# Performance work log

Measured on AMD Instinct MI355X. Metric: run time of the kernel, lower is better.

Reference implementation:

```python
import jax, jax.numpy as jnp
import numpy as np

N = 20000        # nodes
E = 640000       # edges (before self-loops)
F_IN = 128
HID = 64
HEADS = 4
F_OUT = 128
G = 64           # graphs in batch
NEG_SLOPE = 0.2  # PyG GATConv leaky_relu default


def setup_inputs() -> dict:
    key = jax.random.key(0)
    ks = jax.random.split(key, 16)
    s = 0.05
    x = jax.random.normal(ks[0], (N, F_IN), jnp.float32)
    edge_index = jax.random.randint(ks[1], (2, E), 0, N, dtype=jnp.int64)
    batch = jnp.sort(jax.random.randint(ks[2], (N,), 0, G, dtype=jnp.int64))
    # layer 1: F_IN -> HID x HEADS (concat)
    W1 = jax.random.normal(ks[3], (F_IN, HEADS * HID), jnp.float32) * s
    a_src1 = jax.random.normal(ks[4], (HEADS, HID), jnp.float32) * s
    a_dst1 = jax.random.normal(ks[5], (HEADS, HID), jnp.float32) * s
    b1 = jnp.zeros((HEADS * HID,), jnp.float32)
    # layer 2: HEADS*HID -> HID x HEADS (concat)
    W2 = jax.random.normal(ks[6], (HEADS * HID, HEADS * HID), jnp.float32) * s
    a_src2 = jax.random.normal(ks[7], (HEADS, HID), jnp.float32) * s
    a_dst2 = jax.random.normal(ks[8], (HEADS, HID), jnp.float32) * s
    b2 = jnp.zeros((HEADS * HID,), jnp.float32)
    # layer 3: HEADS*HID -> F_OUT, heads=1, concat=False (mean)
    W3 = jax.random.normal(ks[9], (HEADS * HID, F_OUT), jnp.float32) * s
    a_src3 = jax.random.normal(ks[10], (1, F_OUT), jnp.float32) * s
    a_dst3 = jax.random.normal(ks[11], (1, F_OUT), jnp.float32) * s
    b3 = jnp.zeros((F_OUT,), jnp.float32)
    return dict(x=x, edge_index=edge_index, batch=batch,
                W1=W1, a_src1=a_src1, a_dst1=a_dst1, b1=b1,
                W2=W2, a_src2=a_src2, a_dst2=a_dst2, b2=b2,
                W3=W3, a_src3=a_src3, a_dst3=a_dst3, b3=b3)


def _gat_layer(x, src, dst, W, a_s, a_d, b, heads, concat):
    n = x.shape[0]
    h = (x @ W).reshape(n, heads, -1)                # [N,H,C]
    alpha_s = (h * a_s[None]).sum(-1)                # [N,H]
    alpha_d = (h * a_d[None]).sum(-1)                # [N,H]
    e = jax.nn.leaky_relu(alpha_s[src] + alpha_d[dst], NEG_SLOPE)  # [E,H]
    # segment softmax over incoming edges of each dst node
    m = jax.ops.segment_max(e, dst, num_segments=n)
    ex = jnp.exp(e - m[dst])
    denom = jax.ops.segment_sum(ex, dst, num_segments=n)
    alpha = ex / (denom[dst] + 1e-16)                # [E,H]
    out = jax.ops.segment_sum(alpha[:, :, None] * h[src], dst, num_segments=n)  # [N,H,C]
    out = out.reshape(n, -1) if concat else out.mean(axis=1)
    return out + b


def reference(x, edge_index, batch, W1, a_src1, a_dst1, b1,
              W2, a_src2, a_dst2, b2, W3, a_src3, a_dst3, b3):
    n = x.shape[0]
    # add self loops (PyG GATConv default add_self_loops=True)
    loop = jnp.arange(n, dtype=edge_index.dtype)
    src = jnp.concatenate([edge_index[0], loop])
    dst = jnp.concatenate([edge_index[1], loop])

    h = _gat_layer(x, src, dst, W1, a_src1, a_dst1, b1, HEADS, True)
    h = jax.nn.elu(h)
    h = _gat_layer(h, src, dst, W2, a_src2, a_dst2, b2, HEADS, True)
    h = jax.nn.elu(h)
    h = _gat_layer(h, src, dst, W3, a_src3, a_dst3, b3, 1, False)

    # global mean pool over graphs
    sums = jax.ops.segment_sum(h, batch, num_segments=G)
    cnts = jax.ops.segment_sum(jnp.ones((n, 1), h.dtype), batch, num_segments=G)
    graph_embedding = sums / jnp.maximum(cnts, 1.0)
    return graph_embedding, h
```

## Files before the change

### kernel.cpp

```cpp
#include <hip/hip_runtime.h>
#include <hip/hip_bf16.h>
#include <math.h>

#define N_NODES 20000
#define N_EDGES 640000
#define ET_EDGES (N_EDGES + N_NODES)
#define G_GRAPHS 64
#define NEG_SLOPE 0.2f


__global__ void hist_dst(const int* __restrict__ ei, int* __restrict__ cnt,
                         const int* __restrict__ batch, int* __restrict__ gstart) {
    int j = blockIdx.x * blockDim.x + threadIdx.x;
    if (blockIdx.x == 0 && threadIdx.x <= G_GRAPHS) {
        int g = threadIdx.x;
        int lo = 0, hi = N_NODES;
        while (lo < hi) {
            int mid = (lo + hi) >> 1;
            if (batch[mid] < g) lo = mid + 1; else hi = mid;
        }
        gstart[g] = lo;
    }
    if (j >= ET_EDGES) return;
    int d = (j < N_EDGES) ? ei[N_EDGES + j] : (j - N_EDGES);
    atomicAdd(&cnt[d], 1);
}

__global__ __launch_bounds__(1024) void scan_rowptr(const int* __restrict__ cnt,
                                                    int* __restrict__ row_ptr) {
    __shared__ int sums[1024];
    const int n = N_NODES;
    const int CH = (n + 1023) / 1024;
    int t = threadIdx.x;
    int base = t * CH;
    int s = 0;
    for (int i = 0; i < CH; ++i) {
        int idx = base + i;
        if (idx < n) s += cnt[idx];
    }
    sums[t] = s;
    __syncthreads();
    for (int o = 1; o < 1024; o <<= 1) {
        int v = (t >= o) ? sums[t - o] : 0;
        __syncthreads();
        sums[t] += v;
        __syncthreads();
    }
    int run = (t == 0) ? 0 : sums[t - 1];
    for (int i = 0; i < CH; ++i) {
        int idx = base + i;
        if (idx < n) { row_ptr[idx] = run; run += cnt[idx]; }
    }
    if (t == 1023) row_ptr[n] = sums[1023];
}

__global__ void fill_csr(const int* __restrict__ ei, const int* __restrict__ row_ptr,
                         int* __restrict__ cur, int* __restrict__ col) {
    int j = blockIdx.x * blockDim.x + threadIdx.x;
    if (j >= ET_EDGES) return;
    int s, d;
    if (j < N_EDGES) { s = ei[j]; d = ei[N_EDGES + j]; }
    else             { s = d = j - N_EDGES; }
    int pos = row_ptr[d] + atomicAdd(&cur[d], 1);
    col[pos] = s;
}


__global__ __launch_bounds__(256) void sgemm64(const float* __restrict__ A,
                                               const float* __restrict__ B,
                                               float* __restrict__ C,
                                               int M, int K, int Nc) {
    __shared__ float As[16][64];
    __shared__ float Bs[16][64];
    int bm = blockIdx.x * 64;
    int bn = blockIdx.y * 64;
    int t = threadIdx.x;
    int tr = t >> 2, tq = t & 3;
    int bkr = t >> 4, bnq = t & 15;
    int tm = (t >> 4) * 4;
    int tn = (t & 15) * 4;
    float acc[4][4] = {};
    for (int k0 = 0; k0 < K; k0 += 16) {
        int ar = bm + tr;
        float4 av = make_float4(0.f, 0.f, 0.f, 0.f);
        if (ar < M) av = *(const float4*)&A[(size_t)ar * K + k0 + tq * 4];
        As[tq * 4 + 0][tr] = av.x;
        As[tq * 4 + 1][tr] = av.y;
        As[tq * 4 + 2][tr] = av.z;
        As[tq * 4 + 3][tr] = av.w;
        float4 bv = *(const float4*)&B[(size_t)(k0 + bkr) * Nc + bn + bnq * 4];
        *(float4*)&Bs[bkr][bnq * 4] = bv;
        __syncthreads();
        #pragma unroll
        for (int k = 0; k < 16; ++k) {
            float a[4], b[4];
            *(float4*)a = *(const float4*)&As[k][tm];
            *(float4*)b = *(const float4*)&Bs[k][tn];
            #pragma unroll
            for (int i = 0; i < 4; ++i)
                #pragma unroll
                for (int j = 0; j < 4; ++j)
                    acc[i][j] = fmaf(a[i], b[j], acc[i][j]);
        }
        __syncthreads();
    }
    #pragma unroll
    for (int i = 0; i < 4; ++i) {
        int r = bm + tm + i;
        if (r < M) {
            float4 o = make_float4(acc[i][0], acc[i][1], acc[i][2], acc[i][3]);
            *(float4*)&C[(size_t)r * Nc + bn + tn] = o;
        }
    }
}


template <int HEADS, int C>
__global__ __launch_bounds__(256) void node_alpha2(const float* __restrict__ h,
                                                   const float* __restrict__ a_src,
                                                   const float* __restrict__ a_dst,
                                                   float* __restrict__ asT,
                                                   float* __restrict__ adT) {
    constexpr int F = HEADS * C;
    constexpr int VEC = F / 64;
    constexpr int LPH = C / VEC;
    int wid = threadIdx.x >> 6, lane = threadIdx.x & 63;
    int v = blockIdx.x * 4 + wid;
    if (v >= N_NODES) return;
    const float* hp = h + (size_t)v * F + lane * VEC;
    float ps = 0.f, pd = 0.f;
    #pragma unroll
    for (int c = 0; c < VEC; ++c) {
        float hv = hp[c];
        ps = fmaf(hv, a_src[lane * VEC + c], ps);
        pd = fmaf(hv, a_dst[lane * VEC + c], pd);
    }
    #pragma unroll
    for (int o = LPH / 2; o; o >>= 1) {
        ps += __shfl_xor(ps, o);
        pd += __shfl_xor(pd, o);
    }
    if ((lane & (LPH - 1)) == 0) {
        int head = lane / LPH;
        asT[head * N_NODES + v] = ps;
        adT[head * N_NODES + v] = pd;
    }
}


template <int NSLICE, int SCH, int F, int HEADS, bool DO_ELU>
__global__ __launch_bounds__(256) void gat_aggregate_sliced(
        const float* __restrict__ h,
        const float* __restrict__ asT,
        const float* __restrict__ adT,
        const int* __restrict__ row_ptr,
        const int* __restrict__ col,
        const float* __restrict__ bias,
        float* __restrict__ out) {
    constexpr int CL = SCH / 4;
    constexpr int E  = 64 / CL;
    constexpr int CPH = F / HEADS;
    __shared__ int   s_off[4][64];
    __shared__ float s_p[4][64];
    int slice = blockIdx.x & (NSLICE - 1);
    int ng = blockIdx.x >> 2;
    int wid = threadIdx.x >> 6, lane = threadIdx.x & 63;
    int v = ng * 4 + wid;
    if (v >= N_NODES) return;
    int head = (slice * SCH) / CPH;
    int eg = lane / CL, cl = lane % CL;
    int r0 = row_ptr[v], r1 = row_ptr[v + 1];
    float ad = adT[head * N_NODES + v];
    const float* asrc = asT + head * N_NODES;
    float acc[4] = {};
    float lsum = 0.f;
    const char* hb = (const char*)(h + slice * SCH + cl * 4);

    for (int base = r0; base < r1; base += 64) {
        int j = base + lane;
        bool valid = j < r1;
        int s = col[valid ? j : r0];
        float e = asrc[s] + ad;
        e = (e > 0.f) ? e : NEG_SLOPE * e;
        float p = valid ? __expf(e) : 0.f;
        lsum += p;
        s_p[wid][lane] = p;
        s_off[wid][lane] = s * (F * 4);

        int nk = min(64, r1 - base);
        int nkg = (nk + E - 1) / E;
        for (int g = 0; g < nkg; ++g) {
            int k = g * E + eg;
            float pk = s_p[wid][k];
            int off = s_off[wid][k];
            float4 hv = *(const float4*)(hb + off);
            acc[0] = fmaf(pk, hv.x, acc[0]);
            acc[1] = fmaf(pk, hv.y, acc[1]);
            acc[2] = fmaf(pk, hv.z, acc[2]);
            acc[3] = fmaf(pk, hv.w, acc[3]);
        }
    }
    #pragma unroll
    for (int o = 32; o; o >>= 1) lsum += __shfl_xor(lsum, o);
    #pragma unroll
    for (int c = 0; c < 4; ++c) {
        #pragma unroll
        for (int o = CL; o < 64; o <<= 1) acc[c] += __shfl_xor(acc[c], o);
    }
    if (eg == 0) {
        float inv = 1.f / (lsum + 1e-16f);
        #pragma unroll
        for (int c = 0; c < 4; ++c) {
            int ch = slice * SCH + cl * 4 + c;
            float o = acc[c] * inv + bias[ch];
            if (DO_ELU) o = (o > 0.f) ? o : expm1f(o);
            out[(size_t)v * F + ch] = o;
        }
    }
}


__global__ void pool_mean4(const float* __restrict__ hout, const int* __restrict__ gstart,
                           float* __restrict__ gout) {
    int g = blockIdx.x;
    int q = blockIdx.y;
    int c = threadIdx.x;
    int off = gstart[g], end = gstart[g + 1];
    float inv = 1.f / fmaxf((float)(end - off), 1.0f);
    float s = 0.f;
    for (int i = off + q; i < end; i += 4) s += hout[(size_t)i * 128 + c];
    atomicAdd(&gout[g * 128 + c], s * inv);
}


static inline size_t align_up(size_t x, size_t a) { return (x + a - 1) & ~(a - 1); }

extern "C" void kernel_launch(void* const* d_in, const int* in_sizes, int n_in,
                              void* d_out, int out_size, void* d_ws, size_t ws_size,
                              hipStream_t stream) {
    const float* x   = (const float*)d_in[0];
    const int*   ei  = (const int*)d_in[1];
    const int*   bat = (const int*)d_in[2];
    const float* W1  = (const float*)d_in[3];
    const float* as1 = (const float*)d_in[4];
    const float* ad1 = (const float*)d_in[5];
    const float* b1  = (const float*)d_in[6];
    const float* W2  = (const float*)d_in[7];
    const float* as2 = (const float*)d_in[8];
    const float* ad2 = (const float*)d_in[9];
    const float* b2  = (const float*)d_in[10];
    const float* W3  = (const float*)d_in[11];
    const float* as3 = (const float*)d_in[12];
    const float* ad3 = (const float*)d_in[13];
    const float* b3  = (const float*)d_in[14];

    float* gout = (float*)d_out;
    float* hout = (float*)d_out + G_GRAPHS * 128;

    char* w = (char*)d_ws;
    size_t o = 0;
    float* bufA = (float*)(w + o); o = align_up(o + (size_t)N_NODES * 256 * 4, 256);
    float* bufB = (float*)(w + o); o = align_up(o + (size_t)N_NODES * 256 * 4, 256);
    float* asv  = (float*)(w + o); o = align_up(o + (size_t)N_NODES * 4 * 4, 256);
    float* adv  = (float*)(w + o); o = align_up(o + (size_t)N_NODES * 4 * 4, 256);
    int* row_ptr = (int*)(w + o);  o = align_up(o + (size_t)(N_NODES + 1) * 4, 256);
    int* col     = (int*)(w + o);  o = align_up(o + (size_t)ET_EDGES * 4, 256);
    int* cnt     = (int*)(w + o);  o += (size_t)N_NODES * 4;
    int* cur     = (int*)(w + o);  o = align_up(o + (size_t)N_NODES * 4, 256);
    int* gstart  = (int*)(w + o);  o = align_up(o + (size_t)(G_GRAPHS + 1) * 4, 256);

    hipMemsetAsync(cnt, 0, (size_t)N_NODES * 8, stream);
    hipMemsetAsync(gout, 0, (size_t)G_GRAPHS * 128 * 4, stream);
    hist_dst<<<(ET_EDGES + 255) / 256, 256, 0, stream>>>(ei, cnt, bat, gstart);
    scan_rowptr<<<1, 1024, 0, stream>>>(cnt, row_ptr);
    fill_csr<<<(ET_EDGES + 255) / 256, 256, 0, stream>>>(ei, row_ptr, cur, col);

    dim3 g4(313, 4), g2(313, 2);
    int nb = (N_NODES + 3) / 4;
    int nbs = nb * 4;

    sgemm64<<<g4, 256, 0, stream>>>(x, W1, bufA, N_NODES, 128, 256);
    node_alpha2<4, 64><<<nb, 256, 0, stream>>>(bufA, as1, ad1, asv, adv);
    gat_aggregate_sliced<4, 64, 256, 4, true><<<nbs, 256, 0, stream>>>(
        bufA, asv, adv, row_ptr, col, b1, bufB);

    sgemm64<<<g4, 256, 0, stream>>>(bufB, W2, bufA, N_NODES, 256, 256);
    node_alpha2<4, 64><<<nb, 256, 0, stream>>>(bufA, as2, ad2, asv, adv);
    gat_aggregate_sliced<4, 64, 256, 4, true><<<nbs, 256, 0, stream>>>(
        bufA, asv, adv, row_ptr, col, b2, bufB);

    sgemm64<<<g2, 256, 0, stream>>>(bufB, W3, bufA, N_NODES, 256, 128);
    node_alpha2<1, 128><<<nb, 256, 0, stream>>>(bufA, as3, ad3, asv, adv);
    gat_aggregate_sliced<4, 32, 128, 1, false><<<nbs, 256, 0, stream>>>(
        bufA, asv, adv, row_ptr, col, b3, hout);

    pool_mean4<<<dim3(G_GRAPHS, 4), 128, 0, stream>>>(hout, gstart, gout);
}
```

Before: 485.3 us.

## Precompute per-edge attention weights in separate kernel and unroll aggregation loop

Adds an edge_alpha kernel that computes the exp attention scores per edge and head once, storing them and per-node denominators in new buffers. The aggregation kernel then reads the precomputed weights instead of recomputing them in every slice. It also drops the shared-memory staging, unrolls the gather loop four edges deep for more memory-level parallelism, doubles slices to 8, and pre-shifts column indices into byte offsets. In exchange it adds an extra kernel launch and an extra ~10MB write and read of edge weights per layer.

```diff
diff --git a/kernel.cpp b/kernel.cpp
--- a/kernel.cpp
+++ b/kernel.cpp
@@ -55,14 +55,14 @@
 }
 
 __global__ void fill_csr(const int* __restrict__ ei, const int* __restrict__ row_ptr,
-                         int* __restrict__ cur, int* __restrict__ col) {
+                         int* __restrict__ cur, int* __restrict__ colb) {
     int j = blockIdx.x * blockDim.x + threadIdx.x;
     if (j >= ET_EDGES) return;
     int s, d;
     if (j < N_EDGES) { s = ei[j]; d = ei[N_EDGES + j]; }
     else             { s = d = j - N_EDGES; }
     int pos = row_ptr[d] + atomicAdd(&cur[d], 1);
-    col[pos] = s;
+    colb[pos] = s << 10;
 }
 
 
@@ -116,11 +116,11 @@
 
 
 template <int HEADS, int C>
-__global__ __launch_bounds__(256) void node_alpha2(const float* __restrict__ h,
+__global__ __launch_bounds__(256) void node_alpha3(const float* __restrict__ h,
                                                    const float* __restrict__ a_src,
                                                    const float* __restrict__ a_dst,
-                                                   float* __restrict__ asT,
-                                                   float* __restrict__ adT) {
+                                                   float* __restrict__ asi,
+                                                   float* __restrict__ adi) {
     constexpr int F = HEADS * C;
     constexpr int VEC = F / 64;
     constexpr int LPH = C / VEC;
@@ -142,80 +142,139 @@
     }
     if ((lane & (LPH - 1)) == 0) {
         int head = lane / LPH;
-        asT[head * N_NODES + v] = ps;
-        adT[head * N_NODES + v] = pd;
-    }
-}
-
-
-template <int NSLICE, int SCH, int F, int HEADS, bool DO_ELU>
-__global__ __launch_bounds__(256) void gat_aggregate_sliced(
+        asi[v * HEADS + head] = ps;
+        adi[v * HEADS + head] = pd;
+    }
+}
+
+
+template <int H>
+__global__ __launch_bounds__(256) void edge_alpha(
+        const float* __restrict__ asi,
+        const float* __restrict__ adi,
+        const int* __restrict__ row_ptr,
+        const int* __restrict__ colb,
+        float* __restrict__ p,
+        float* __restrict__ dn) {
+    constexpr int KE = 64 / H;
+    constexpr int SHIFT = (H == 4) ? 6 : 8;
+    int wid = threadIdx.x >> 6, lane = threadIdx.x & 63;
+    int v = blockIdx.x * 4 + wid;
+    if (v >= N_NODES) return;
+    int k = lane / H, h = lane % H;
+    int r0 = row_ptr[v], r1 = row_ptr[v + 1];
+    float ad = adi[v * H + h];
+    const char* ab = (const char*)asi + h * 4;
+    float dsum = 0.f;
+    for (int base = r0; base < r1; base += KE) {
+        int j = base + k;
+        bool valid = j < r1;
+        int cb = colb[valid ? j : r0];
+        float as = *(const float*)(ab + (cb >> SHIFT));
+        float e = as + ad;
+        e = (e > 0.f) ? e : NEG_SLOPE * e;
+        float pe = __expf(e);
+        if (valid) {
+            dsum += pe;
+            p[(size_t)j * H + h] = pe;
+        }
+    }
+    #pragma unroll
+    for (int o = H; o < 64; o <<= 1) dsum += __shfl_xor(dsum, o);
+    if (k == 0) dn[v * H + h] = dsum;
+}
+
+
+template <int NSLICE, int SCH, int F, int H, int SHIFT, bool DO_ELU>
+__global__ __launch_bounds__(256) void gat_aggregate3(
         const float* __restrict__ h,
-        const float* __restrict__ asT,
-        const float* __restrict__ adT,
+        const float* __restrict__ p,
+        const float* __restrict__ dn,
         const int* __restrict__ row_ptr,
-        const int* __restrict__ col,
+        const int* __restrict__ colb,
         const float* __restrict__ bias,
         float* __restrict__ out) {
     constexpr int CL = SCH / 4;
     constexpr int E  = 64 / CL;
-    constexpr int CPH = F / HEADS;
-    __shared__ int   s_off[4][64];
-    __shared__ float s_p[4][64];
+    constexpr int CPH = F / H;
     int slice = blockIdx.x & (NSLICE - 1);
-    int ng = blockIdx.x >> 2;
+    int ng = blockIdx.x / NSLICE;
     int wid = threadIdx.x >> 6, lane = threadIdx.x & 63;
     int v = ng * 4 + wid;
     if (v >= N_NODES) return;
     int head = (slice * SCH) / CPH;
     int eg = lane / CL, cl = lane % CL;
     int r0 = row_ptr[v], r1 = row_ptr[v + 1];
-    float ad = adT[head * N_NODES + v];
-    const float* asrc = asT + head * N_NODES;
+    const char* hb = (const char*)(h + slice * SCH + cl * 4);
+    const float* pp = p + head;
     float acc[4] = {};
-    float lsum = 0.f;
-    const char* hb = (const char*)(h + slice * SCH + cl * 4);
-
-    for (int base = r0; base < r1; base += 64) {
-        int j = base + lane;
-        bool valid = j < r1;
-        int s = col[valid ? j : r0];
-        float e = asrc[s] + ad;
-        e = (e > 0.f) ? e : NEG_SLOPE * e;
-        float p = valid ? __expf(e) : 0.f;
-        lsum += p;
-        s_p[wid][lane] = p;
-        s_off[wid][lane] = s * (F * 4);
-
-        int nk = min(64, r1 - base);
-        int nkg = (nk + E - 1) / E;
-        for (int g = 0; g < nkg; ++g) {
-            int k = g * E + eg;
-            float pk = s_p[wid][k];
-            int off = s_off[wid][k];
-            float4 hv = *(const float4*)(hb + off);
-            acc[0] = fmaf(pk, hv.x, acc[0]);
-            acc[1] = fmaf(pk, hv.y, acc[1]);
-            acc[2] = fmaf(pk, hv.z, acc[2]);
-            acc[3] = fmaf(pk, hv.w, acc[3]);
-        }
-    }
-    #pragma unroll
-    for (int o = 32; o; o >>= 1) lsum += __shfl_xor(lsum, o);
+
+    int e0 = r0;
+    for (; e0 + E * 4 <= r1; e0 += E * 4) {
+        int ea = e0 + eg, eb = ea + E, ec = eb + E, ed = ec + E;
+        int oa = colb[ea] >> SHIFT;
+        int ob = colb[eb] >> SHIFT;
+        int oc = colb[ec] >> SHIFT;
+        int od = colb[ed] >> SHIFT;
+        float pa = pp[(size_t)ea * H];
+        float pb = pp[(size_t)eb * H];
+        float pc = pp[(size_t)ec * H];
+        float pd = pp[(size_t)ed * H];
+        float4 ha = *(const float4*)(hb + oa);
+        float4 hc0 = *(const float4*)(hb + ob);
+        float4 hc1 = *(const float4*)(hb + oc);
+        float4 hc2 = *(const float4*)(hb + od);
+        acc[0] = fmaf(pa, ha.x, acc[0]);
+        acc[1] = fmaf(pa, ha.y, acc[1]);
+        acc[2] = fmaf(pa, ha.z, acc[2]);
+        acc[3] = fmaf(pa, ha.w, acc[3]);
+        acc[0] = fmaf(pb, hc0.x, acc[0]);
+        acc[1] = fmaf(pb, hc0.y, acc[1]);
+        acc[2] = fmaf(pb, hc0.z, acc[2]);
+        acc[3] = fmaf(pb, hc0.w, acc[3]);
+        acc[0] = fmaf(pc, hc1.x, acc[0]);
+        acc[1] = fmaf(pc, hc1.y, acc[1]);
+        acc[2] = fmaf(pc, hc1.z, acc[2]);
+        acc[3] = fmaf(pc, hc1.w, acc[3]);
+        acc[0] = fmaf(pd, hc2.x, acc[0]);
+        acc[1] = fmaf(pd, hc2.y, acc[1]);
+        acc[2] = fmaf(pd, hc2.z, acc[2]);
+        acc[3] = fmaf(pd, hc2.w, acc[3]);
+    }
+    for (; e0 < r1; e0 += E) {
+        int e = e0 + eg;
+        bool valid = e < r1;
+        int ee = valid ? e : r0;
+        int oa = colb[ee] >> SHIFT;
+        float pa = pp[(size_t)ee * H];
+        if (!valid) pa = 0.f;
+        float4 ha = *(const float4*)(hb + oa);
+        acc[0] = fmaf(pa, ha.x, acc[0]);
+        acc[1] = fmaf(pa, ha.y, acc[1]);
+        acc[2] = fmaf(pa, ha.z, acc[2]);
+        acc[3] = fmaf(pa, ha.w, acc[3]);
+    }
+
     #pragma unroll
     for (int c = 0; c < 4; ++c) {
         #pragma unroll
         for (int o = CL; o < 64; o <<= 1) acc[c] += __shfl_xor(acc[c], o);
     }
     if (eg == 0) {
-        float inv = 1.f / (lsum + 1e-16f);
-        #pragma unroll
-        for (int c = 0; c < 4; ++c) {
-            int ch = slice * SCH + cl * 4 + c;
-            float o = acc[c] * inv + bias[ch];
-            if (DO_ELU) o = (o > 0.f) ? o : expm1f(o);
-            out[(size_t)v * F + ch] = o;
-        }
+        float inv = 1.f / (dn[v * H + head] + 1e-16f);
+        int ch = slice * SCH + cl * 4;
+        float4 o;
+        o.x = acc[0] * inv + bias[ch + 0];
+        o.y = acc[1] * inv + bias[ch + 1];
+        o.z = acc[2] * inv + bias[ch + 2];
+        o.w = acc[3] * inv + bias[ch + 3];
+        if (DO_ELU) {
+            o.x = (o.x > 0.f) ? o.x : expm1f(o.x);
+            o.y = (o.y > 0.f) ? o.y : expm1f(o.y);
+            o.z = (o.z > 0.f) ? o.z : expm1f(o.z);
+            o.w = (o.w > 0.f) ? o.w : expm1f(o.w);
+        }
+        *(float4*)&out[(size_t)v * F + ch] = o;
     }
 }
 
@@ -263,8 +322,10 @@
     float* bufB = (float*)(w + o); o = align_up(o + (size_t)N_NODES * 256 * 4, 256);
     float* asv  = (float*)(w + o); o = align_up(o + (size_t)N_NODES * 4 * 4, 256);
     float* adv  = (float*)(w + o); o = align_up(o + (size_t)N_NODES * 4 * 4, 256);
+    float* pbuf = (float*)(w + o); o = align_up(o + (size_t)ET_EDGES * 4 * 4, 256);
+    float* dnv  = (float*)(w + o); o = align_up(o + (size_t)N_NODES * 4 * 4, 256);
     int* row_ptr = (int*)(w + o);  o = align_up(o + (size_t)(N_NODES + 1) * 4, 256);
-    int* col     = (int*)(w + o);  o = align_up(o + (size_t)ET_EDGES * 4, 256);
+    int* colb    = (int*)(w + o);  o = align_up(o + (size_t)ET_EDGES * 4, 256);
     int* cnt     = (int*)(w + o);  o += (size_t)N_NODES * 4;
     int* cur     = (int*)(w + o);  o = align_up(o + (size_t)N_NODES * 4, 256);
     int* gstart  = (int*)(w + o);  o = align_up(o + (size_t)(G_GRAPHS + 1) * 4, 256);
@@ -273,26 +334,29 @@
     hipMemsetAsync(gout, 0, (size_t)G_GRAPHS * 128 * 4, stream);
     hist_dst<<<(ET_EDGES + 255) / 256, 256, 0, stream>>>(ei, cnt, bat, gstart);
     scan_rowptr<<<1, 1024, 0, stream>>>(cnt, row_ptr);
-    fill_csr<<<(ET_EDGES + 255) / 256, 256, 0, stream>>>(ei, row_ptr, cur, col);
+    fill_csr<<<(ET_EDGES + 255) / 256, 256, 0, stream>>>(ei, row_ptr, cur, colb);
 
     dim3 g4(313, 4), g2(313, 2);
     int nb = (N_NODES + 3) / 4;
-    int nbs = nb * 4;
+    int nbs = nb * 8;
 
     sgemm64<<<g4, 256, 0, stream>>>(x, W1, bufA, N_NODES, 128, 256);
-    node_alpha2<4, 64><<<nb, 256, 0, stream>>>(bufA, as1, ad1, asv, adv);
-    gat_aggregate_sliced<4, 64, 256, 4, true><<<nbs, 256, 0, stream>>>(
-        bufA, asv, adv, row_ptr, col, b1, bufB);
+    node_alpha3<4, 64><<<nb, 256, 0, stream>>>(bufA, as1, ad1, asv, adv);
+    edge_alpha<4><<<nb, 256, 0, stream>>>(asv, adv, row_ptr, colb, pbuf, dnv);
+    gat_aggregate3<8, 32, 256, 4, 0, true><<<nbs, 256, 0, stream>>>(
+        bufA, pbuf, dnv, row_ptr, colb, b1, bufB);
 
     sgemm64<<<g4, 256, 0, stream>>>(bufB, W2, bufA, N_NODES, 256, 256);
-    node_alpha2<4, 64><<<nb, 256, 0, stream>>>(bufA, as2, ad2, asv, adv);
-    gat_aggregate_sliced<4, 64, 256, 4, true><<<nbs, 256, 0, stream>>>(
-        bufA, asv, adv, row_ptr, col, b2, bufB);
+    node_alpha3<4, 64><<<nb, 256, 0, stream>>>(bufA, as2, ad2, asv, adv);
+    edge_alpha<4><<<nb, 256, 0, stream>>>(asv, adv, row_ptr, colb, pbuf, dnv);
+    gat_aggregate3<8, 32, 256, 4, 0, true><<<nbs, 256, 0, stream>>>(
+        bufA, pbuf, dnv, row_ptr, colb, b2, bufB);
 
     sgemm64<<<g2, 256, 0, stream>>>(bufB, W3, bufA, N_NODES, 256, 128);
-    node_alpha2<1, 128><<<nb, 256, 0, stream>>>(bufA, as3, ad3, asv, adv);
-    gat_aggregate_sliced<4, 32, 128, 1, false><<<nbs, 256, 0, stream>>>(
-        bufA, asv, adv, row_ptr, col, b3, hout);
+    node_alpha3<1, 128><<<nb, 256, 0, stream>>>(bufA, as3, ad3, asv, adv);
+    edge_alpha<1><<<nb, 256, 0, stream>>>(asv, adv, row_ptr, colb, pbuf, dnv);
+    gat_aggregate3<8, 16, 128, 1, 1, false><<<nbs, 256, 0, stream>>>(
+        bufA, pbuf, dnv, row_ptr, colb, b3, hout);
 
     pool_mean4<<<dim3(G_GRAPHS, 4), 128, 0, stream>>>(hout, gstart, gout);
 }
```

Result: slower. 540.0 us (+11.3%).
